# Kernel tuning notes

Hardware: AMD Instinct MI355X
Metric: run time of the kernel (lower is better)

The kernel has to match this reference:

```python
import jax, jax.numpy as jnp
import numpy as np

T, B, E, H = 1024, 4, 1024, 16
Dh = E // H
NEG_INF = float('-inf')


def setup_inputs() -> dict:
    key = jax.random.key(0)
    k1, k2, k3, k4 = jax.random.split(key, 4)
    return {
        'fwd_x': jax.random.normal(k1, (T, B, E), jnp.float32),
        'bwd_x': jax.random.normal(k2, (T, B, E), jnp.float32),
        'in_proj_weight': jax.random.normal(k3, (3 * E, E), jnp.float32) * 0.02,
        'in_proj_bias': jnp.zeros((3 * E,), jnp.float32),
        'out_w': jax.random.normal(k4, (E, E), jnp.float32) * 0.02,
        'out_b': jnp.zeros((E,), jnp.float32),
    }


def reference(fwd_x, bwd_x, in_proj_weight, in_proj_bias, out_w, out_b):
    t, b, e = fwd_x.shape
    s = 2 * t
    dtype = fwd_x.dtype
    zeros = jnp.zeros((1, b, e), dtype)
    # padded_fwd_x[0:t] -> [0, fwd_x[:-1]]; padded_bwd_x[1:t+1] -> [bwd_x[1:], 0]
    q_in = jnp.concatenate([zeros, fwd_x[:-1]], 0) + jnp.concatenate([bwd_x[1:], zeros], 0)
    kv = jnp.concatenate([fwd_x, bwd_x], 0)  # [s, b, e]

    wq, wk, wv = in_proj_weight[:e], in_proj_weight[e:2 * e], in_proj_weight[2 * e:]
    bq, bk, bv = in_proj_bias[:e], in_proj_bias[e:2 * e], in_proj_bias[2 * e:]
    q = (q_in @ wq.T + bq).reshape(t, b, H, Dh)
    k = (kv @ wk.T + bk).reshape(s, b, H, Dh)
    v = (kv @ wv.T + bv).reshape(s, b, H, Dh)

    # NOTE: original module never applies self.scaling in forward -- keep unscaled.
    attn_weights = jnp.einsum('tbhd,sbhd->bhts', q, k)  # [b, H, t, s]

    # mask_curr_state=True: allowed keys are j < i (fwd half) or j > i + t (bwd half)
    i = jnp.arange(t)[:, None]
    j = jnp.arange(s)[None, :]
    allowed = (j >= i + t + 1) | (j <= i - 1)
    mask_bias = jnp.where(allowed, 0.0, NEG_INF).astype(dtype)
    attn_weights = attn_weights + mask_bias[None, None]

    probs = jax.nn.softmax(attn_weights.astype(jnp.float32), axis=-1).astype(dtype)

    attn = jnp.einsum('bhts,sbhd->tbhd', probs, v).reshape(t, b, e)
    attn = attn @ out_w.T + out_b
    avg_weights = probs.mean(axis=1)  # [b, t, s]
    return attn, avg_weights
```

## Files before the change

kernel.cpp:

```cpp
#include <hip/hip_runtime.h>

typedef unsigned short u16;
typedef __attribute__((ext_vector_type(8))) short short8;
typedef __attribute__((ext_vector_type(4))) float f32x4;

#define SM_SHIFT 24.0f

__device__ __forceinline__ u16 f2b(float f) {
  unsigned u = __float_as_uint(f);
  unsigned r = (u + 0x7FFFu + ((u >> 16) & 1u)) >> 16;
  return (u16)r;
}

__device__ __forceinline__ void gload16(const u16* g, u16* l) {
  __builtin_amdgcn_global_load_lds((const __attribute__((address_space(1))) void*)g,
                                   (__attribute__((address_space(3))) void*)l, 16, 0, 0);
}

__device__ __forceinline__ void cast4(const float* __restrict__ src,
                                      u16* __restrict__ dst, int gid) {
  float4 v = *(const float4*)(src + (gid << 2));
  ushort4 o; o.x = f2b(v.x); o.y = f2b(v.y); o.z = f2b(v.z); o.w = f2b(v.w);
  *(ushort4*)(dst + (gid << 2)) = o;
}

__global__ __launch_bounds__(256) void prep_all(const float* __restrict__ fwd,
                                                const float* __restrict__ bwd,
                                                const float* __restrict__ w_in,
                                                const float* __restrict__ w_out,
                                                u16* __restrict__ qin,
                                                u16* __restrict__ kvf,
                                                u16* __restrict__ kvb,
                                                u16* __restrict__ wbf,
                                                u16* __restrict__ wobf) {
  const int blk = blockIdx.x, tid = threadIdx.x;
  if (blk < 4096) {
    int gid = blk * 256 + tid;
    int n = gid >> 8;
    int e4 = (gid & 255) << 2;
    int t = n >> 2, b = n & 3;
    float4 acc = make_float4(0.f, 0.f, 0.f, 0.f);
    if (t > 0) {
      float4 v = *(const float4*)(fwd + (((t - 1) * 4 + b) << 10) + e4);
      acc.x += v.x; acc.y += v.y; acc.z += v.z; acc.w += v.w;
    }
    if (t < 1023) {
      float4 v = *(const float4*)(bwd + (((t + 1) * 4 + b) << 10) + e4);
      acc.x += v.x; acc.y += v.y; acc.z += v.z; acc.w += v.w;
    }
    ushort4 o; o.x = f2b(acc.x); o.y = f2b(acc.y); o.z = f2b(acc.z); o.w = f2b(acc.w);
    *(ushort4*)(qin + (n << 10) + e4) = o;
  } else if (blk < 8192) {
    cast4(fwd, kvf, (blk - 4096) * 256 + tid);
  } else if (blk < 12288) {
    cast4(bwd, kvb, (blk - 8192) * 256 + tid);
  } else if (blk < 15360) {
    cast4(w_in, wbf, (blk - 12288) * 256 + tid);
  } else {
    cast4(w_out, wobf, (blk - 15360) * 256 + tid);
  }
}

template <int MODE, int NB>
__global__ __launch_bounds__(256) void gemm_bt(const u16* __restrict__ A,
                                               const u16* __restrict__ W,
                                               const float* __restrict__ bias,
                                               void* __restrict__ outp,
                                               void* __restrict__ outp2) {
  __shared__ u16 At[NB][128 * 64];
  __shared__ u16 Wt[NB][128 * 64];
  const int m0 = blockIdx.x << 7, n0 = blockIdx.y << 7;
  const int tid = threadIdx.x;
  const int lane = tid & 63, wid = tid >> 6;
  const int wm = (wid >> 1) << 6, wn = (wid & 1) << 6;
  const int lr = lane & 15, lg = lane >> 4;
  const int srow = lane >> 3, scol = (lane & 7) << 3;
  const int swc = ((lane & 7) ^ srow) << 3;
  f32x4 acc[4][4] = {};
  auto stage = [&](int buf, int k0) {
#pragma unroll
    for (int it = 0; it < 4; it++) {
      int row = (it * 4 + wid) * 8 + srow;
      gload16(&A[(m0 + row) * 1024 + k0 + swc], &At[buf][row * 64 + scol]);
      gload16(&W[(n0 + row) * 1024 + k0 + swc], &Wt[buf][row * 64 + scol]);
    }
  };
  auto compute = [&](int buf) {
#pragma unroll
    for (int kk = 0; kk < 64; kk += 32) {
      short8 af[4], bf[4];
#pragma unroll
      for (int i = 0; i < 4; i++) {
        int co = (((kk >> 3) + lg) ^ (lr & 7)) << 3;
        af[i] = *(const short8*)&At[buf][(wm + i * 16 + lr) * 64 + co];
        bf[i] = *(const short8*)&Wt[buf][(wn + i * 16 + lr) * 64 + co];
      }
#pragma unroll
      for (int i = 0; i < 4; i++)
#pragma unroll
        for (int j = 0; j < 4; j++)
          acc[i][j] = __builtin_amdgcn_mfma_f32_16x16x32_bf16(af[i], bf[j], acc[i][j], 0, 0, 0);
    }
  };
  if constexpr (NB == 2) {
    stage(0, 0);
    __syncthreads();
    for (int step = 0; step < 16; ++step) {
      const int cur = step & 1;
      if (step < 15) stage(cur ^ 1, (step + 1) << 6);
      compute(cur);
      __syncthreads();
    }
  } else {
    for (int step = 0; step < 16; ++step) {
      __syncthreads();
      stage(0, step << 6);
      __syncthreads();
      compute(0);
    }
  }
#pragma unroll
  for (int i = 0; i < 4; i++) {
#pragma unroll
    for (int j = 0; j < 4; j++) {
      int n = n0 + wn + j * 16 + lr;
      float bv = bias[n];
#pragma unroll
      for (int r = 0; r < 4; r++) {
        int m = m0 + wm + i * 16 + lg * 4 + r;
        float v = acc[i][j][r] + bv;
        if (MODE == 3) {
          ((float*)outp)[m * 1024 + n] = v;
        } else if (MODE == 0) {
          int tb = m & 3, ts = m >> 2, hh = n >> 6, d = n & 63;
          ((u16*)outp)[((tb * 16 + hh) * 1024 + ts) * 64 + d] = f2b(v);
        } else {
          u16* ob = (n0 < 1024) ? (u16*)outp : (u16*)outp2;
          int nl = (n0 < 1024) ? n : n - 1024;
          int tb = m & 3, ts = m >> 2, hh = nl >> 6, d = nl & 63;
          ob[((tb * 16 + hh) * 2048 + ts) * 64 + d] = f2b(v);
        }
      }
    }
  }
}

__global__ __launch_bounds__(256) void transpose_v(const u16* __restrict__ v,
                                                   u16* __restrict__ vt) {
  __shared__ u16 L[64 * 66];
  const int blk = blockIdx.x;
  const int bh = blk >> 5, s0 = (blk & 31) << 6;
  const int tid = threadIdx.x;
  const u16* src = v + ((size_t)bh * 2048 + s0) * 64;
  u16* dst = vt + (size_t)bh * 64 * 2048 + s0;
#pragma unroll
  for (int it = 0; it < 2; ++it) {
    int idx = it * 256 + tid;
    int sl = idx >> 3, dc = (idx & 7) << 3;
    short8 v8 = *(const short8*)&src[sl * 64 + dc];
#pragma unroll
    for (int e = 0; e < 8; ++e)
      L[(dc + e) * 66 + sl] = (u16)v8[e];
  }
  __syncthreads();
#pragma unroll
  for (int it = 0; it < 2; ++it) {
    int idx = it * 256 + tid;
    int dr = idx >> 3, sc = (idx & 7) << 3;
    *(short8*)&dst[(size_t)dr * 2048 + sc] = *(const short8*)&L[dr * 66 + sc];
  }
}

__global__ __launch_bounds__(256) void attn_fwd(const u16* __restrict__ qb,
                                                const u16* __restrict__ kb,
                                                const u16* __restrict__ vtb,
                                                u16* __restrict__ attn_bf,
                                                float* __restrict__ st_il) {
  __shared__ u16 Kt[64 * 64];
  __shared__ u16 Vt[64 * 64];
  __shared__ u16 Pt[4][16 * 72];
  const int g = blockIdx.x;
  const int L = ((g & 7) << 7) | (g >> 3);
  const int t0 = (L & 15) << 6;
  const int h = (L >> 4) & 15;
  const int b = L >> 8;
  const int tid = threadIdx.x, lane = tid & 63, w = tid >> 6;
  const int lr = lane & 15, lg = lane >> 4;
  const int bh = b * 16 + h;
  const int sw0 = ((lg ^ (lr & 7)) << 3);
  const int sw1 = sw0 ^ 32;
  const u16* qrow = qb + ((bh << 10) + t0 + (w << 4) + lr) * 64;
  short8 qf0 = *(const short8*)&qrow[lg * 8];
  short8 qf1 = *(const short8*)&qrow[32 + lg * 8];
  const u16* kbase = kb + (size_t)(bh << 11) * 64;
  const u16* vbase = vtb + (size_t)(bh << 6) * 2048;
  f32x4 acc[4] = {};
  f32x4 accl = {};
  const int n1 = (t0 >> 6) + 1;
  const int grow = lane >> 3, gcol = (lane & 7) << 3;
  short8 ones;
#pragma unroll
  for (int j = 0; j < 8; ++j) ones[j] = (short)0x3F80;
  for (int ti = 0; ti < 17; ++ti) {
    const int s0 = (ti < n1) ? (ti << 6) : (t0 + 1024 + ((ti - n1) << 6));
    __syncthreads();
#pragma unroll
    for (int it = 0; it < 2; ++it) {
      int row = (it * 4 + w) * 8 + grow;
      int swc = (((lane & 7) ^ (row & 7)) << 3);
      gload16(&kbase[(size_t)(s0 + row) * 64 + swc], &Kt[row * 64 + gcol]);
      gload16(&vbase[(size_t)row * 2048 + s0 + swc], &Vt[row * 64 + gcol]);
    }
    __syncthreads();
    float pv[4][4];
#pragma unroll
    for (int c = 0; c < 4; c++) {
      f32x4 sc = {};
      short8 kf0 = *(const short8*)&Kt[(c * 16 + lr) * 64 + sw0];
      short8 kf1 = *(const short8*)&Kt[(c * 16 + lr) * 64 + sw1];
      sc = __builtin_amdgcn_mfma_f32_16x16x32_bf16(qf0, kf0, sc, 0, 0, 0);
      sc = __builtin_amdgcn_mfma_f32_16x16x32_bf16(qf1, kf1, sc, 0, 0, 0);
      int j = s0 + c * 16 + lr;
#pragma unroll
      for (int r = 0; r < 4; r++) {
        int i = t0 + (w << 4) + lg * 4 + r;
        float e = __expf(sc[r] - SM_SHIFT);
        pv[c][r] = ((j < i) || (j > i + 1024)) ? e : 0.f;
      }
    }
#pragma unroll
    for (int c = 0; c < 4; c++)
#pragma unroll
      for (int r = 0; r < 4; r++)
        Pt[w][(lg * 4 + r) * 72 + c * 16 + lr] = f2b(pv[c][r]);
    short8 pf0 = *(const short8*)&Pt[w][lr * 72 + lg * 8];
    short8 pf1 = *(const short8*)&Pt[w][lr * 72 + 32 + lg * 8];
    accl = __builtin_amdgcn_mfma_f32_16x16x32_bf16(pf0, ones, accl, 0, 0, 0);
    accl = __builtin_amdgcn_mfma_f32_16x16x32_bf16(pf1, ones, accl, 0, 0, 0);
#pragma unroll
    for (int dd = 0; dd < 4; dd++) {
      short8 vf0 = *(const short8*)&Vt[(dd * 16 + lr) * 64 + sw0];
      short8 vf1 = *(const short8*)&Vt[(dd * 16 + lr) * 64 + sw1];
      acc[dd] = __builtin_amdgcn_mfma_f32_16x16x32_bf16(pf0, vf0, acc[dd], 0, 0, 0);
      acc[dd] = __builtin_amdgcn_mfma_f32_16x16x32_bf16(pf1, vf1, acc[dd], 0, 0, 0);
    }
  }
  float inv[4];
#pragma unroll
  for (int r = 0; r < 4; r++) inv[r] = 1.f / accl[r];
  const int trow = t0 + (w << 4) + lg * 4;
#pragma unroll
  for (int dd = 0; dd < 4; dd++)
#pragma unroll
    for (int r = 0; r < 4; r++)
      attn_bf[((trow + r) * 4 + b) * 1024 + h * 64 + dd * 16 + lr] = f2b(acc[dd][r] * inv[r]);
#pragma unroll
  for (int r = 0; r < 4; r++)
    if (lr == r)
      st_il[(bh << 10) + trow + r] = inv[r];
}

__global__ __launch_bounds__(256) void attn_avg(const u16* __restrict__ qb,
                                                const u16* __restrict__ kb,
                                                const float* __restrict__ st_il,
                                                float* __restrict__ avg) {
  __shared__ u16 Kt[128 * 64];
  __shared__ float Si[16][64];
  const int g = blockIdx.x;
  const int L = ((g & 7) << 7) | (g >> 3);
  const int s0 = (L & 15) << 7;
  const int t0 = ((L >> 4) & 15) << 6;
  const int b = L >> 8;
  const int tid = threadIdx.x, lane = tid & 63, w = tid >> 6;
  const int lr = lane & 15, lg = lane >> 4;
  const int trow = t0 + (w << 4) + lg * 4;
  float* obase = avg + (size_t)b * (1024 * 2048);
  if ((s0 > t0 + 62) && (s0 + 127 < t0 + 1025)) {
#pragma unroll
    for (int c = 0; c < 8; c++)
#pragma unroll
      for (int r = 0; r < 4; r++)
        obase[(trow + r) * 2048 + s0 + c * 16 + lr] = 0.f;
    return;
  }
  for (int i = tid; i < 1024; i += 256) {
    int hh = i >> 6, tt = i & 63;
    Si[hh][tt] = st_il[(((b << 4) + hh) << 10) + t0 + tt];
  }
  const int sw0 = ((lg ^ (lr & 7)) << 3);
  const int sw1 = sw0 ^ 32;
  const int grow = lane >> 3, gcol = (lane & 7) << 3;
  const int srr = (w << 4) + lg * 4;
  float accv[8][4] = {};
  for (int h = 0; h < 16; h++) {
    const int bh = (b << 4) + h;
    __syncthreads();
    {
      const u16* kb_h = kb + ((size_t)((bh << 11) + s0)) * 64;
#pragma unroll
      for (int it = 0; it < 4; ++it) {
        int row = (it * 4 + w) * 8 + grow;
        int swc = (((lane & 7) ^ (row & 7)) << 3);
        gload16(&kb_h[(size_t)row * 64 + swc], &Kt[row * 64 + gcol]);
      }
    }
    const u16* qrow = qb + ((bh << 10) + t0 + (w << 4) + lr) * 64;
    short8 qf0 = *(const short8*)&qrow[lg * 8];
    short8 qf1 = *(const short8*)&qrow[32 + lg * 8];
    float ih[4];
#pragma unroll
    for (int r = 0; r < 4; r++) ih[r] = Si[h][srr + r];
    __syncthreads();
#pragma unroll
    for (int c = 0; c < 8; c++) {
      int c0 = s0 + (c << 4);
      if (c0 >= t0 + 63 && c0 <= t0 + 1009) continue;
      f32x4 sc = {};
      short8 kf0 = *(const short8*)&Kt[(c * 16 + lr) * 64 + sw0];
      short8 kf1 = *(const short8*)&Kt[(c * 16 + lr) * 64 + sw1];
      sc = __builtin_amdgcn_mfma_f32_16x16x32_bf16(qf0, kf0, sc, 0, 0, 0);
      sc = __builtin_amdgcn_mfma_f32_16x16x32_bf16(qf1, kf1, sc, 0, 0, 0);
      int j = c0 + lr;
#pragma unroll
      for (int r = 0; r < 4; r++) {
        int i = t0 + (w << 4) + lg * 4 + r;
        if ((j < i) || (j > i + 1024))
          accv[c][r] += __expf(sc[r] - SM_SHIFT) * ih[r];
      }
    }
  }
#pragma unroll
  for (int c = 0; c < 8; c++)
#pragma unroll
    for (int r = 0; r < 4; r++)
      obase[(trow + r) * 2048 + s0 + c * 16 + lr] = accv[c][r] * 0.0625f;
}

extern "C" void kernel_launch(void* const* d_in, const int* in_sizes, int n_in,
                              void* d_out, int out_size, void* d_ws, size_t ws_size,
                              hipStream_t stream) {
  const float* fwd   = (const float*)d_in[0];
  const float* bwd   = (const float*)d_in[1];
  const float* w_in  = (const float*)d_in[2];
  const float* b_in  = (const float*)d_in[3];
  const float* w_out = (const float*)d_in[4];
  const float* b_out = (const float*)d_in[5];

  char* ws = (char*)d_ws;
  u16*  q_in_bf = (u16*)(ws);
  u16*  kv_bf   = (u16*)(ws + 8388608);
  u16*  vt_bf   = (u16*)(ws + 8388608);
  u16*  w_bf    = (u16*)(ws + 25165824);
  u16*  wo_bf   = (u16*)(ws + 31457280);
  u16*  q_bf    = (u16*)(ws + 33554432);
  u16*  k_bf    = (u16*)(ws + 41943040);
  u16*  v_tmp   = (u16*)(ws + 58720256);
  u16*  attn_bf = (u16*)(ws + 75497472);
  float* st_il  = (float*)(ws + 83886080);

  float* out_attn = (float*)d_out;
  float* out_avg  = (float*)d_out + 4194304;

  prep_all<<<16384, 256, 0, stream>>>(fwd, bwd, w_in, w_out, q_in_bf, kv_bf,
                                      kv_bf + 4194304, w_bf, wo_bf);

  gemm_bt<0, 2><<<dim3(32, 8), 256, 0, stream>>>(q_in_bf, w_bf, b_in,
                                                 (void*)q_bf, nullptr);
  gemm_bt<1, 1><<<dim3(64, 16), 256, 0, stream>>>(kv_bf, w_bf + 1048576,
                                                  b_in + 1024, (void*)k_bf,
                                                  (void*)v_tmp);
  transpose_v<<<2048, 256, 0, stream>>>(v_tmp, vt_bf);

  attn_fwd<<<1024, 256, 0, stream>>>(q_bf, k_bf, vt_bf, attn_bf, st_il);

  gemm_bt<3, 2><<<dim3(32, 8), 256, 0, stream>>>(attn_bf, wo_bf, b_out,
                                                 (void*)out_attn, nullptr);

  attn_avg<<<1024, 256, 0, stream>>>(q_bf, k_bf, st_il, out_avg);
}
```

Before: 204.9 us.

## Double-buffer K tiles in attn_avg and remap GEMM blocks per XCD

attn_avg now prefetches the next head's K tile into a second LDS buffer while computing the current head, which removes one barrier per iteration and overlaps global loads with MFMA work. The GEMM kernels switch to a 1D grid whose block index is remapped so that each of the 8 XCDs gets a contiguous group of M tiles, aiming for better L2 reuse of the A and W tiles. The cost is twice the LDS for K in attn_avg, which may lower occupancy.

```diff
diff --git a/kernel.cpp b/kernel.cpp
--- a/kernel.cpp
+++ b/kernel.cpp
@@ -61,7 +61,7 @@
   }
 }
 
-template <int MODE, int NB>
+template <int MODE, int NB, int MTX, int NTT>
 __global__ __launch_bounds__(256) void gemm_bt(const u16* __restrict__ A,
                                                const u16* __restrict__ W,
                                                const float* __restrict__ bias,
@@ -69,7 +69,10 @@
                                                void* __restrict__ outp2) {
   __shared__ u16 At[NB][128 * 64];
   __shared__ u16 Wt[NB][128 * 64];
-  const int m0 = blockIdx.x << 7, n0 = blockIdx.y << 7;
+  const int x = blockIdx.x & 7, local = blockIdx.x >> 3;
+  const int mt = x * MTX + (local % MTX);
+  const int nt = local / MTX;
+  const int m0 = mt << 7, n0 = nt << 7;
   const int tid = threadIdx.x;
   const int lane = tid & 63, wid = tid >> 6;
   const int wm = (wid >> 1) << 6, wn = (wid & 1) << 6;
@@ -264,7 +267,7 @@
                                                 const u16* __restrict__ kb,
                                                 const float* __restrict__ st_il,
                                                 float* __restrict__ avg) {
-  __shared__ u16 Kt[128 * 64];
+  __shared__ u16 Kt[2][128 * 64];
   __shared__ float Si[16][64];
   const int g = blockIdx.x;
   const int L = ((g & 7) << 7) | (g >> 3);
@@ -291,33 +294,35 @@
   const int sw1 = sw0 ^ 32;
   const int grow = lane >> 3, gcol = (lane & 7) << 3;
   const int srr = (w << 4) + lg * 4;
+  auto stage = [&](int buf, int hh) {
+    const u16* kb_h = kb + ((size_t)(((b << 4) + hh) << 11) + s0) * 64;
+#pragma unroll
+    for (int it = 0; it < 4; ++it) {
+      int row = (it * 4 + w) * 8 + grow;
+      int swc = (((lane & 7) ^ (row & 7)) << 3);
+      gload16(&kb_h[(size_t)row * 64 + swc], &Kt[buf][row * 64 + gcol]);
+    }
+  };
+  stage(0, 0);
+  __syncthreads();
   float accv[8][4] = {};
   for (int h = 0; h < 16; h++) {
+    const int cur = h & 1;
+    if (h < 15) stage(cur ^ 1, h + 1);
     const int bh = (b << 4) + h;
-    __syncthreads();
-    {
-      const u16* kb_h = kb + ((size_t)((bh << 11) + s0)) * 64;
-#pragma unroll
-      for (int it = 0; it < 4; ++it) {
-        int row = (it * 4 + w) * 8 + grow;
-        int swc = (((lane & 7) ^ (row & 7)) << 3);
-        gload16(&kb_h[(size_t)row * 64 + swc], &Kt[row * 64 + gcol]);
-      }
-    }
     const u16* qrow = qb + ((bh << 10) + t0 + (w << 4) + lr) * 64;
     short8 qf0 = *(const short8*)&qrow[lg * 8];
     short8 qf1 = *(const short8*)&qrow[32 + lg * 8];
     float ih[4];
 #pragma unroll
     for (int r = 0; r < 4; r++) ih[r] = Si[h][srr + r];
-    __syncthreads();
 #pragma unroll
     for (int c = 0; c < 8; c++) {
       int c0 = s0 + (c << 4);
       if (c0 >= t0 + 63 && c0 <= t0 + 1009) continue;
       f32x4 sc = {};
-      short8 kf0 = *(const short8*)&Kt[(c * 16 + lr) * 64 + sw0];
-      short8 kf1 = *(const short8*)&Kt[(c * 16 + lr) * 64 + sw1];
+      short8 kf0 = *(const short8*)&Kt[cur][(c * 16 + lr) * 64 + sw0];
+      short8 kf1 = *(const short8*)&Kt[cur][(c * 16 + lr) * 64 + sw1];
       sc = __builtin_amdgcn_mfma_f32_16x16x32_bf16(qf0, kf0, sc, 0, 0, 0);
       sc = __builtin_amdgcn_mfma_f32_16x16x32_bf16(qf1, kf1, sc, 0, 0, 0);
       int j = c0 + lr;
@@ -328,6 +333,7 @@
           accv[c][r] += __expf(sc[r] - SM_SHIFT) * ih[r];
       }
     }
+    __syncthreads();
   }
 #pragma unroll
   for (int c = 0; c < 8; c++)
@@ -364,17 +370,17 @@
   prep_all<<<16384, 256, 0, stream>>>(fwd, bwd, w_in, w_out, q_in_bf, kv_bf,
                                       kv_bf + 4194304, w_bf, wo_bf);
 
-  gemm_bt<0, 2><<<dim3(32, 8), 256, 0, stream>>>(q_in_bf, w_bf, b_in,
-                                                 (void*)q_bf, nullptr);
-  gemm_bt<1, 1><<<dim3(64, 16), 256, 0, stream>>>(kv_bf, w_bf + 1048576,
-                                                  b_in + 1024, (void*)k_bf,
-                                                  (void*)v_tmp);
+  gemm_bt<0, 2, 4, 8><<<256, 256, 0, stream>>>(q_in_bf, w_bf, b_in,
+                                               (void*)q_bf, nullptr);
+  gemm_bt<1, 1, 8, 16><<<1024, 256, 0, stream>>>(kv_bf, w_bf + 1048576,
+                                                 b_in + 1024, (void*)k_bf,
+                                                 (void*)v_tmp);
   transpose_v<<<2048, 256, 0, stream>>>(v_tmp, vt_bf);
 
   attn_fwd<<<1024, 256, 0, stream>>>(q_bf, k_bf, vt_bf, attn_bf, st_il);
 
-  gemm_bt<3, 2><<<dim3(32, 8), 256, 0, stream>>>(attn_bf, wo_bf, b_out,
-                                                 (void*)out_attn, nullptr);
+  gemm_bt<3, 2, 4, 8><<<256, 256, 0, stream>>>(attn_bf, wo_bf, b_out,
+                                               (void*)out_attn, nullptr);
 
   attn_avg<<<1024, 256, 0, stream>>>(q_bf, k_bf, st_il, out_avg);
 }
```

Result: no change. 201.9 us (-1.4%).
